# Performance work log

Hardware: AMD Instinct MI355X
Metric: run time of the kernel (lower is better)

## Reference

```python
import jax, jax.numpy as jnp
import numpy as np

E, K = 16, 4          # n_experts, top_k
C, H = 2048, 3584     # d_model, ffn_hidden
B, T = 2, 512
STD = 0.02


def setup_inputs() -> dict:
    key = jax.random.key(0)
    ks = jax.random.split(key, 5)
    x = jax.random.normal(ks[0], (B, T, C), jnp.float32)
    W_up = jax.random.normal(ks[1], (E, H, C), jnp.float32) * STD
    W_gate = jax.random.normal(ks[2], (E, H, C), jnp.float32) * STD
    W_down = jax.random.normal(ks[3], (E, C, H), jnp.float32) * STD
    gate_inp = jax.random.normal(ks[4], (E, C), jnp.float32) * STD
    return {"x": x, "W_up": W_up, "W_gate": W_gate, "W_down": W_down,
            "gate_inp": gate_inp}


def reference(x, W_up, W_gate, W_down, gate_inp):
    # x: [B, T, C]
    b, t, c = x.shape
    xf = x.reshape(b * t, c)                                  # [N, C]
    logits = xf @ gate_inp.T                                  # [N, E]
    topv, topi = jax.lax.top_k(logits, K)                     # [N, K]
    w = jax.nn.softmax(topv.astype(jnp.float32), axis=-1).astype(x.dtype)
    n = xf.shape[0]
    # Dense combine weights: zero for unselected experts -> identical math
    # to the original per-token gather, without the [N,K,H,C] blowup.
    dense_w = jnp.zeros((n, E), x.dtype).at[jnp.arange(n)[:, None], topi].set(w)
    u = jnp.einsum('nc,ehc->neh', xf, W_up)                   # [N, E, H]
    g = jnp.einsum('nc,ehc->neh', xf, W_gate)                 # [N, E, H]
    h = jax.nn.silu(g) * u                                    # SwiGLU
    y = jnp.einsum('neh,ech,ne->nc', h, W_down, dense_w)      # weighted combine
    return y.reshape(b, t, c)
```

## Files before the change

kernel.cpp:

```cpp
#include <hip/hip_runtime.h>
#include <math.h>

#define NTOK   1024
#define EXP    16
#define TOPK   4
#define DMODEL 2048
#define DFFN   3584
#define HT_TILES 56
#define CT_TILES 32
#define NSLOT  4096
#define MCH    64
#define NCHMAX 80

typedef __attribute__((ext_vector_type(8))) short bf16x8;
typedef __attribute__((ext_vector_type(4))) float f32x4;

#define O_COUNTS 0
#define O_BASE   256
#define O_CURSOR 512
#define O_CHT    1024
#define O_TOPI   4096
#define O_TOPW   (O_TOPI + 16384)
#define O_TOK    (O_TOPW + 16384)
#define O_WGT    (O_TOK + 16384)
#define O_SLOTNK (O_WGT + 16384)
#define O_XG     (O_SLOTNK + 16384)
#define O_HBUF   (O_XG + (size_t)NSLOT*DMODEL*2)

#define VMW(N) asm volatile("s_waitcnt vmcnt(" #N ")" ::: "memory")
#define LKW0() asm volatile("s_waitcnt lgkmcnt(0)" ::: "memory")
#define BAR()  __builtin_amdgcn_s_barrier()

__device__ __forceinline__ unsigned short f2b_rne(float f) {
  unsigned u = __builtin_bit_cast(unsigned, f);
  u += 0x7FFFu + ((u >> 16) & 1u);
  return (unsigned short)(u >> 16);
}
__device__ __forceinline__ float b2f(unsigned short h) {
  unsigned u = ((unsigned)h) << 16;
  return __builtin_bit_cast(float, u);
}
__device__ __forceinline__ unsigned pk2(float lo, float hi) {
  unsigned r;
  asm("v_cvt_pk_bf16_f32 %0, %1, %2" : "=v"(r) : "v"(lo), "v"(hi));
  return r;
}
__device__ __forceinline__ bf16x8 pack8(float4 a, float4 b) {
  union { unsigned u[4]; bf16x8 v; } r;
  r.u[0] = pk2(a.x, a.y); r.u[1] = pk2(a.z, a.w);
  r.u[2] = pk2(b.x, b.y); r.u[3] = pk2(b.z, b.w);
  return r.v;
}

__device__ __forceinline__ void gl16(const unsigned short* g, unsigned short* l) {
  __builtin_amdgcn_global_load_lds(
      (const __attribute__((address_space(1))) void*)g,
      (__attribute__((address_space(3))) void*)l, 16, 0, 0);
}

__device__ __forceinline__ bf16x8 ld_frag(const unsigned short* lds, int row, int chunk) {
  return *(const bf16x8*)(lds + row*64 + ((chunk ^ (row & 7)) * 8));
}

__global__ void k_zero(int* counts, int* cursor) {
  int t = threadIdx.x;
  if (t < EXP) { counts[t] = 0; cursor[t] = 0; }
}

__global__ void k_gate(const float* __restrict__ x, const float* __restrict__ gi,
                       int* __restrict__ topi, float* __restrict__ topw,
                       int* __restrict__ counts) {
  int n = blockIdx.x;
  int lane = threadIdx.x & 63, wave = threadIdx.x >> 6;
  __shared__ float lg[EXP];
  const float4* xr = (const float4*)(x + (size_t)n * DMODEL);
  #pragma unroll
  for (int i = 0; i < 4; ++i) {
    int e = wave * 4 + i;
    const float4* gr = (const float4*)(gi + (size_t)e * DMODEL);
    float s = 0.f;
    #pragma unroll
    for (int j = 0; j < 8; ++j) {
      float4 a = xr[j*64 + lane];
      float4 b = gr[j*64 + lane];
      s += a.x*b.x + a.y*b.y + a.z*b.z + a.w*b.w;
    }
    #pragma unroll
    for (int off = 32; off; off >>= 1) s += __shfl_xor(s, off);
    if (lane == 0) lg[e] = s;
  }
  __syncthreads();
  if (threadIdx.x == 0) {
    float v[EXP];
    #pragma unroll
    for (int j = 0; j < EXP; ++j) v[j] = lg[j];
    int bi[TOPK]; float bv[TOPK];
    #pragma unroll
    for (int k = 0; k < TOPK; ++k) {
      float best = -3.4e38f; int bidx = 0;
      for (int j = 0; j < EXP; ++j) if (v[j] > best) { best = v[j]; bidx = j; }
      bv[k] = best; bi[k] = bidx; v[bidx] = -3.4e38f;
    }
    float m = bv[0], ss = 0.f, w[TOPK];
    #pragma unroll
    for (int k = 0; k < TOPK; ++k) { w[k] = expf(bv[k] - m); ss += w[k]; }
    #pragma unroll
    for (int k = 0; k < TOPK; ++k) {
      topi[n*TOPK + k] = bi[k];
      topw[n*TOPK + k] = w[k] / ss;
      atomicAdd(&counts[bi[k]], 1);
    }
  }
}

__global__ void k_prefix(const int* __restrict__ counts, int* __restrict__ basep,
                         int* __restrict__ chtab) {
  if (threadIdx.x == 0) {
    int acc = 0;
    for (int e = 0; e < EXP; ++e) { basep[e] = acc; acc += counts[e]; }
    int c = 0;
    for (int e = 0; e < EXP; ++e) {
      int nm = (counts[e] + MCH - 1) / MCH;
      for (int m = 0; m < nm; ++m) { chtab[1 + c] = (e << 8) | m; ++c; }
    }
    chtab[0] = c;
    for (; c < NCHMAX; ++c) chtab[1 + c] = -1;
  }
}

__global__ void k_scatter(const int* __restrict__ topi, const float* __restrict__ topw,
                          const int* __restrict__ basep, int* __restrict__ cursor,
                          int* __restrict__ tok, float* __restrict__ wgt,
                          int* __restrict__ slotnk) {
  int n = blockIdx.x * blockDim.x + threadIdx.x;
  if (n >= NTOK) return;
  #pragma unroll
  for (int k = 0; k < TOPK; ++k) {
    int e = topi[n*TOPK + k];
    int pos = atomicAdd(&cursor[e], 1);
    int slot = basep[e] + pos;
    tok[slot] = n;
    wgt[slot] = topw[n*TOPK + k];
    slotnk[n*TOPK + k] = slot;
  }
}

__global__ void k_gather(const float* __restrict__ x, const int* __restrict__ tok,
                         unsigned short* __restrict__ xg) {
  int slot = blockIdx.x;
  int t = tok[slot];
  int c0 = threadIdx.x * 8;
  const float* src = x + (size_t)t * DMODEL + c0;
  float4 a = *(const float4*)(src);
  float4 b = *(const float4*)(src + 4);
  uint4 o = {pk2(a.x, a.y), pk2(a.z, a.w), pk2(b.x, b.y), pk2(b.z, b.w)};
  *(uint4*)(xg + (size_t)slot * DMODEL + c0) = o;
}

#define UG_STEP(XSC, XSN, PC, PN, KC) do {                                     \
    BAR();                                                                     \
    int kn_ = (KC) + 1; if (kn_ > DMODEL/64 - 1) kn_ = DMODEL/64 - 1;          \
    const float* pu_ = wu_row + kn_*64;                                        \
    const float* pg_ = wg_row + kn_*64;                                        \
    float4 r0_ = *(const float4*)(pu_);                                        \
    float4 r1_ = *(const float4*)(pu_ + 4);                                    \
    float4 r2_ = *(const float4*)(pu_ + 32);                                   \
    float4 r3_ = *(const float4*)(pu_ + 36);                                   \
    float4 r4_ = *(const float4*)(pg_);                                        \
    float4 r5_ = *(const float4*)(pg_ + 4);                                    \
    float4 r6_ = *(const float4*)(pg_ + 32);                                   \
    float4 r7_ = *(const float4*)(pg_ + 36);                                   \
    _Pragma("unroll")                                                          \
    for (int i_ = 0; i_ < 2; ++i_)                                             \
      gl16(bx[i_] + kn_*64, (XSN) + (wave*2 + i_)*8*64);                       \
    VMW(10);                                                                   \
    BAR();                                                                     \
    __builtin_amdgcn_s_setprio(1);                                             \
    _Pragma("unroll")                                                          \
    for (int kk_ = 0; kk_ < 2; ++kk_) {                                        \
      int chunk_ = kk_*4 + (lane >> 4);                                        \
      _Pragma("unroll")                                                        \
      for (int t_ = 0; t_ < 4; ++t_) {                                         \
        bf16x8 a_ = ld_frag((XSC), t_*16 + col, chunk_);                       \
        ua[t_] = __builtin_amdgcn_mfma_f32_16x16x32_bf16(a_, PC[kk_],   ua[t_], 0, 0, 0); \
        ga[t_] = __builtin_amdgcn_mfma_f32_16x16x32_bf16(a_, PC[2+kk_], ga[t_], 0, 0, 0); \
      }                                                                        \
    }                                                                          \
    __builtin_amdgcn_s_setprio(0);                                             \
    VMW(2);                                                                    \
    PN[0] = pack8(r0_, r1_); PN[1] = pack8(r2_, r3_);                          \
    PN[2] = pack8(r4_, r5_); PN[3] = pack8(r6_, r7_);                          \
  } while (0)

__global__ __launch_bounds__(256, 4) void k_upgate(
    const unsigned short* __restrict__ xg,
    const float* __restrict__ Wu, const float* __restrict__ Wg,
    const int* __restrict__ counts, const int* __restrict__ basep,
    const int* __restrict__ chtab, const float* __restrict__ wgt,
    unsigned short* __restrict__ hbuf) {
  int bid = blockIdx.x;
  int lb  = (bid & 7) * (NCHMAX*HT_TILES/8) + (bid >> 3);
  int cid = lb % NCHMAX, ht = lb / NCHMAX;
  int ent = chtab[1 + cid];
  if (ent < 0) return;
  int e = ent >> 8, mch = ent & 255;
  int n_e = counts[e], base_e = basep[e], mstart = mch * MCH;

  __shared__ unsigned short xs[2][64*64];
  __shared__ float swgt[MCH];

  int tid = threadIdx.x;
  int lane = tid & 63, wave = tid >> 6;
  int col = lane & 15;
  int kgrp = (lane >> 4) * 8;
  const float* wu_row = Wu + ((size_t)e * DFFN + (size_t)(ht*64 + wave*16 + col)) * DMODEL + kgrp;
  const float* wg_row = Wg + ((size_t)e * DFFN + (size_t)(ht*64 + wave*16 + col)) * DMODEL + kgrp;

  int xrow_lo = lane >> 3;
  int xpc     = lane & 7;
  int swz     = (xpc ^ xrow_lo) * 8;

  const unsigned short* bx[2];
  #pragma unroll
  for (int i = 0; i < 2; ++i) {
    int row = (wave*2 + i)*8 + xrow_lo;
    int slotr = base_e + mstart + row;
    if (slotr > NSLOT-1) slotr = NSLOT-1;
    bx[i] = xg + (size_t)slotr*DMODEL + swz;
  }

  if (tid < MCH) {
    int r = mstart + tid;
    swgt[tid] = (r < n_e) ? wgt[base_e + r] : 0.f;
  }
  LKW0();

  bf16x8 pA[4], pB[4];
  {
    const float* pu_ = wu_row;
    const float* pg_ = wg_row;
    float4 r0 = *(const float4*)(pu_);
    float4 r1 = *(const float4*)(pu_ + 4);
    float4 r2 = *(const float4*)(pu_ + 32);
    float4 r3 = *(const float4*)(pu_ + 36);
    float4 r4 = *(const float4*)(pg_);
    float4 r5 = *(const float4*)(pg_ + 4);
    float4 r6 = *(const float4*)(pg_ + 32);
    float4 r7 = *(const float4*)(pg_ + 36);
    #pragma unroll
    for (int i = 0; i < 2; ++i)
      gl16(bx[i], &xs[0][(wave*2 + i)*8*64]);
    VMW(2);
    pA[0] = pack8(r0, r1); pA[1] = pack8(r2, r3);
    pA[2] = pack8(r4, r5); pA[3] = pack8(r6, r7);
  }

  f32x4 ua[4], ga[4];
  #pragma unroll
  for (int t = 0; t < 4; ++t) { f32x4 z = {0.f,0.f,0.f,0.f}; ua[t] = z; ga[t] = z; }

  #pragma unroll 1
  for (int kc = 0; kc < DMODEL/64; kc += 2) {
    UG_STEP(xs[0], xs[1], pA, pB, kc);
    UG_STEP(xs[1], xs[0], pB, pA, kc + 1);
  }

  #pragma unroll
  for (int t = 0; t < 4; ++t)
    #pragma unroll
    for (int r = 0; r < 4; ++r) {
      int ml = t*16 + (lane >> 4)*4 + r;
      if (mstart + ml < n_e) {
        float u = ua[t][r], g = ga[t][r];
        float hv = u * (g / (1.f + expf(-g))) * swgt[ml];
        int slot = base_e + mstart + ml;
        hbuf[(size_t)slot*DFFN + ht*64 + wave*16 + col] = f2b_rne(hv);
      }
    }
}

#define DN_STEP(XSC, XSN, PC, PN, KC) do {                                     \
    BAR();                                                                     \
    int kn_ = (KC) + 1; if (kn_ > DFFN/64 - 1) kn_ = DFFN/64 - 1;              \
    const float* pd_ = wd_row + kn_*64;                                        \
    float4 r0_ = *(const float4*)(pd_);                                        \
    float4 r1_ = *(const float4*)(pd_ + 4);                                    \
    float4 r2_ = *(const float4*)(pd_ + 32);                                   \
    float4 r3_ = *(const float4*)(pd_ + 36);                                   \
    _Pragma("unroll")                                                          \
    for (int i_ = 0; i_ < 2; ++i_)                                             \
      gl16(bh[i_] + kn_*64, (XSN) + (wave*2 + i_)*8*64);                       \
    VMW(6);                                                                    \
    BAR();                                                                     \
    __builtin_amdgcn_s_setprio(1);                                             \
    _Pragma("unroll")                                                          \
    for (int kk_ = 0; kk_ < 2; ++kk_) {                                        \
      int chunk_ = kk_*4 + (lane >> 4);                                        \
      _Pragma("unroll")                                                        \
      for (int t_ = 0; t_ < 4; ++t_) {                                         \
        bf16x8 a_ = ld_frag((XSC), t_*16 + col, chunk_);                       \
        acc[t_] = __builtin_amdgcn_mfma_f32_16x16x32_bf16(a_, PC[kk_], acc[t_], 0, 0, 0); \
      }                                                                        \
    }                                                                          \
    __builtin_amdgcn_s_setprio(0);                                             \
    VMW(2);                                                                    \
    PN[0] = pack8(r0_, r1_); PN[1] = pack8(r2_, r3_);                          \
  } while (0)

__global__ __launch_bounds__(256, 4) void k_down(
    const unsigned short* __restrict__ hbuf, const float* __restrict__ Wd,
    const int* __restrict__ counts, const int* __restrict__ basep,
    const int* __restrict__ chtab,
    unsigned short* __restrict__ ypart) {
  int bid = blockIdx.x;
  int lb  = (bid & 7) * (NCHMAX*CT_TILES/8) + (bid >> 3);
  int cid = lb % NCHMAX, ct = lb / NCHMAX;
  int ent = chtab[1 + cid];
  if (ent < 0) return;
  int e = ent >> 8, mch = ent & 255;
  int n_e = counts[e], base_e = basep[e], mstart = mch * MCH;

  __shared__ unsigned short hs[2][64*64];

  int tid = threadIdx.x;
  int lane = tid & 63, wave = tid >> 6;
  int col = lane & 15;
  int kgrp = (lane >> 4) * 8;
  const float* wd_row = Wd + ((size_t)e * DMODEL + (size_t)(ct*64 + wave*16 + col)) * DFFN + kgrp;

  int xrow_lo = lane >> 3;
  int xpc     = lane & 7;
  int swz     = (xpc ^ xrow_lo) * 8;

  const unsigned short* bh[2];
  #pragma unroll
  for (int i = 0; i < 2; ++i) {
    int row = (wave*2 + i)*8 + xrow_lo;
    int slotr = base_e + mstart + row;
    if (slotr > NSLOT-1) slotr = NSLOT-1;
    bh[i] = hbuf + (size_t)slotr*DFFN + swz;
  }

  bf16x8 pA[2], pB[2];
  {
    const float* pd_ = wd_row;
    float4 r0 = *(const float4*)(pd_);
    float4 r1 = *(const float4*)(pd_ + 4);
    float4 r2 = *(const float4*)(pd_ + 32);
    float4 r3 = *(const float4*)(pd_ + 36);
    #pragma unroll
    for (int i = 0; i < 2; ++i)
      gl16(bh[i], &hs[0][(wave*2 + i)*8*64]);
    VMW(2);
    pA[0] = pack8(r0, r1); pA[1] = pack8(r2, r3);
  }

  f32x4 acc[4];
  #pragma unroll
  for (int t = 0; t < 4; ++t) { f32x4 z = {0.f,0.f,0.f,0.f}; acc[t] = z; }

  #pragma unroll 1
  for (int hc = 0; hc < DFFN/64; hc += 2) {
    DN_STEP(hs[0], hs[1], pA, pB, hc);
    DN_STEP(hs[1], hs[0], pB, pA, hc + 1);
  }

  #pragma unroll
  for (int t = 0; t < 4; ++t)
    #pragma unroll
    for (int r = 0; r < 4; ++r) {
      int ml = t*16 + (lane >> 4)*4 + r;
      if (mstart + ml < n_e) {
        int slot = base_e + mstart + ml;
        ypart[(size_t)slot*DMODEL + ct*64 + wave*16 + col] = f2b_rne(acc[t][r]);
      }
    }
}

__global__ void k_combine(const unsigned short* __restrict__ ypart,
                          const int* __restrict__ slotnk, float* __restrict__ out) {
  int n = blockIdx.x, tid = threadIdx.x;
  int c0 = tid * 8;
  float acc[8] = {0.f,0.f,0.f,0.f,0.f,0.f,0.f,0.f};
  #pragma unroll
  for (int k = 0; k < TOPK; ++k) {
    int slot = slotnk[n*TOPK + k];
    uint4 v = *(const uint4*)(ypart + (size_t)slot*DMODEL + c0);
    const unsigned short* p = (const unsigned short*)&v;
    #pragma unroll
    for (int j = 0; j < 8; ++j) acc[j] += b2f(p[j]);
  }
  float4 o0 = {acc[0], acc[1], acc[2], acc[3]};
  float4 o1 = {acc[4], acc[5], acc[6], acc[7]};
  *(float4*)(out + (size_t)n*DMODEL + c0)     = o0;
  *(float4*)(out + (size_t)n*DMODEL + c0 + 4) = o1;
}

extern "C" void kernel_launch(void* const* d_in, const int* in_sizes, int n_in,
                              void* d_out, int out_size, void* d_ws, size_t ws_size,
                              hipStream_t stream) {
  const float* x     = (const float*)d_in[0];
  const float* W_up  = (const float*)d_in[1];
  const float* W_gt  = (const float*)d_in[2];
  const float* W_dn  = (const float*)d_in[3];
  const float* g_in  = (const float*)d_in[4];
  float* out = (float*)d_out;
  char* ws = (char*)d_ws;

  int*   counts = (int*)(ws + O_COUNTS);
  int*   basep  = (int*)(ws + O_BASE);
  int*   cursor = (int*)(ws + O_CURSOR);
  int*   chtab  = (int*)(ws + O_CHT);
  int*   topi   = (int*)(ws + O_TOPI);
  float* topw   = (float*)(ws + O_TOPW);
  int*   tok    = (int*)(ws + O_TOK);
  float* wgt    = (float*)(ws + O_WGT);
  int*   slotnk = (int*)(ws + O_SLOTNK);
  unsigned short* xg    = (unsigned short*)(ws + O_XG);
  unsigned short* hbuf  = (unsigned short*)(ws + O_HBUF);
  unsigned short* ypart = xg;

  k_zero   <<<1, 64, 0, stream>>>(counts, cursor);
  k_gate   <<<NTOK, 256, 0, stream>>>(x, g_in, topi, topw, counts);
  k_prefix <<<1, 64, 0, stream>>>(counts, basep, chtab);
  k_scatter<<<4, 256, 0, stream>>>(topi, topw, basep, cursor, tok, wgt, slotnk);
  k_gather <<<NSLOT, 256, 0, stream>>>(x, tok, xg);
  k_upgate <<<NCHMAX*HT_TILES, 256, 0, stream>>>(xg, W_up, W_gt, counts, basep, chtab, wgt, hbuf);
  k_down   <<<NCHMAX*CT_TILES, 256, 0, stream>>>(hbuf, W_dn, counts, basep, chtab, ypart);
  k_combine<<<NTOK, 256, 0, stream>>>(ypart, slotnk, out);
}
```

Baseline: 916.9 us.

## Load activation fragments directly from global into registers, dropping LDS staging and barriers

Both grouped GEMM kernels (up/gate and down) no longer stage the token-activation tile in LDS through global_load_lds with barriers. Each lane now loads its MFMA A fragments straight from global memory into registers, double-buffered at a 32-wide K step. Launch bounds go from 4 to 3 blocks per CU to make room for the extra registers. This removes barrier and LDS traffic, but the four waves of a block now each reload the same activation rows, which adds L2/global traffic and uses smaller, less coalesced loads.

```diff
diff --git a/kernel.cpp b/kernel.cpp
--- a/kernel.cpp
+++ b/kernel.cpp
@@ -27,10 +27,6 @@
 #define O_XG     (O_SLOTNK + 16384)
 #define O_HBUF   (O_XG + (size_t)NSLOT*DMODEL*2)
 
-#define VMW(N) asm volatile("s_waitcnt vmcnt(" #N ")" ::: "memory")
-#define LKW0() asm volatile("s_waitcnt lgkmcnt(0)" ::: "memory")
-#define BAR()  __builtin_amdgcn_s_barrier()
-
 __device__ __forceinline__ unsigned short f2b_rne(float f) {
   unsigned u = __builtin_bit_cast(unsigned, f);
   u += 0x7FFFu + ((u >> 16) & 1u);
@@ -50,16 +46,6 @@
   r.u[0] = pk2(a.x, a.y); r.u[1] = pk2(a.z, a.w);
   r.u[2] = pk2(b.x, b.y); r.u[3] = pk2(b.z, b.w);
   return r.v;
-}
-
-__device__ __forceinline__ void gl16(const unsigned short* g, unsigned short* l) {
-  __builtin_amdgcn_global_load_lds(
-      (const __attribute__((address_space(1))) void*)g,
-      (__attribute__((address_space(3))) void*)l, 16, 0, 0);
-}
-
-__device__ __forceinline__ bf16x8 ld_frag(const unsigned short* lds, int row, int chunk) {
-  return *(const bf16x8*)(lds + row*64 + ((chunk ^ (row & 7)) * 8));
 }
 
 __global__ void k_zero(int* counts, int* cursor) {
@@ -157,42 +143,26 @@
   *(uint4*)(xg + (size_t)slot * DMODEL + c0) = o;
 }
 
-#define UG_STEP(XSC, XSN, PC, PN, KC) do {                                     \
-    BAR();                                                                     \
-    int kn_ = (KC) + 1; if (kn_ > DMODEL/64 - 1) kn_ = DMODEL/64 - 1;          \
-    const float* pu_ = wu_row + kn_*64;                                        \
-    const float* pg_ = wg_row + kn_*64;                                        \
-    float4 r0_ = *(const float4*)(pu_);                                        \
-    float4 r1_ = *(const float4*)(pu_ + 4);                                    \
-    float4 r2_ = *(const float4*)(pu_ + 32);                                   \
-    float4 r3_ = *(const float4*)(pu_ + 36);                                   \
-    float4 r4_ = *(const float4*)(pg_);                                        \
-    float4 r5_ = *(const float4*)(pg_ + 4);                                    \
-    float4 r6_ = *(const float4*)(pg_ + 32);                                   \
-    float4 r7_ = *(const float4*)(pg_ + 36);                                   \
+#define UG_STEP(AC, AN, PUC, PGC, PUN, PGN, KN) do {                           \
+    int o_ = (KN) * 32;                                                        \
+    AN[0] = *(const bf16x8*)(ax[0] + o_);                                      \
+    AN[1] = *(const bf16x8*)(ax[1] + o_);                                      \
+    AN[2] = *(const bf16x8*)(ax[2] + o_);                                      \
+    AN[3] = *(const bf16x8*)(ax[3] + o_);                                      \
+    float4 u0_ = *(const float4*)(wu + o_);                                    \
+    float4 u1_ = *(const float4*)(wu + o_ + 4);                                \
+    float4 g0_ = *(const float4*)(wg + o_);                                    \
+    float4 g1_ = *(const float4*)(wg + o_ + 4);                                \
     _Pragma("unroll")                                                          \
-    for (int i_ = 0; i_ < 2; ++i_)                                             \
-      gl16(bx[i_] + kn_*64, (XSN) + (wave*2 + i_)*8*64);                       \
-    VMW(10);                                                                   \
-    BAR();                                                                     \
-    __builtin_amdgcn_s_setprio(1);                                             \
-    _Pragma("unroll")                                                          \
-    for (int kk_ = 0; kk_ < 2; ++kk_) {                                        \
-      int chunk_ = kk_*4 + (lane >> 4);                                        \
-      _Pragma("unroll")                                                        \
-      for (int t_ = 0; t_ < 4; ++t_) {                                         \
-        bf16x8 a_ = ld_frag((XSC), t_*16 + col, chunk_);                       \
-        ua[t_] = __builtin_amdgcn_mfma_f32_16x16x32_bf16(a_, PC[kk_],   ua[t_], 0, 0, 0); \
-        ga[t_] = __builtin_amdgcn_mfma_f32_16x16x32_bf16(a_, PC[2+kk_], ga[t_], 0, 0, 0); \
-      }                                                                        \
+    for (int t_ = 0; t_ < 4; ++t_) {                                           \
+      ua[t_] = __builtin_amdgcn_mfma_f32_16x16x32_bf16(AC[t_], PUC, ua[t_], 0, 0, 0); \
+      ga[t_] = __builtin_amdgcn_mfma_f32_16x16x32_bf16(AC[t_], PGC, ga[t_], 0, 0, 0); \
     }                                                                          \
-    __builtin_amdgcn_s_setprio(0);                                             \
-    VMW(2);                                                                    \
-    PN[0] = pack8(r0_, r1_); PN[1] = pack8(r2_, r3_);                          \
-    PN[2] = pack8(r4_, r5_); PN[3] = pack8(r6_, r7_);                          \
+    PUN = pack8(u0_, u1_);                                                     \
+    PGN = pack8(g0_, g1_);                                                     \
   } while (0)
 
-__global__ __launch_bounds__(256, 4) void k_upgate(
+__global__ __launch_bounds__(256, 3) void k_upgate(
     const unsigned short* __restrict__ xg,
     const float* __restrict__ Wu, const float* __restrict__ Wg,
     const int* __restrict__ counts, const int* __restrict__ basep,
@@ -200,59 +170,38 @@
     unsigned short* __restrict__ hbuf) {
   int bid = blockIdx.x;
   int lb  = (bid & 7) * (NCHMAX*HT_TILES/8) + (bid >> 3);
-  int cid = lb % NCHMAX, ht = lb / NCHMAX;
+  int ht  = lb / NCHMAX, cid = lb % NCHMAX;
   int ent = chtab[1 + cid];
   if (ent < 0) return;
   int e = ent >> 8, mch = ent & 255;
   int n_e = counts[e], base_e = basep[e], mstart = mch * MCH;
 
-  __shared__ unsigned short xs[2][64*64];
-  __shared__ float swgt[MCH];
-
   int tid = threadIdx.x;
   int lane = tid & 63, wave = tid >> 6;
-  int col = lane & 15;
-  int kgrp = (lane >> 4) * 8;
-  const float* wu_row = Wu + ((size_t)e * DFFN + (size_t)(ht*64 + wave*16 + col)) * DMODEL + kgrp;
-  const float* wg_row = Wg + ((size_t)e * DFFN + (size_t)(ht*64 + wave*16 + col)) * DMODEL + kgrp;
-
-  int xrow_lo = lane >> 3;
-  int xpc     = lane & 7;
-  int swz     = (xpc ^ xrow_lo) * 8;
-
-  const unsigned short* bx[2];
-  #pragma unroll
-  for (int i = 0; i < 2; ++i) {
-    int row = (wave*2 + i)*8 + xrow_lo;
-    int slotr = base_e + mstart + row;
+  int col  = lane & 15;
+  int krow = lane >> 4;
+
+  const unsigned short* ax[4];
+  #pragma unroll
+  for (int t = 0; t < 4; ++t) {
+    int slotr = base_e + mstart + t*16 + col;
     if (slotr > NSLOT-1) slotr = NSLOT-1;
-    bx[i] = xg + (size_t)slotr*DMODEL + swz;
-  }
-
-  if (tid < MCH) {
-    int r = mstart + tid;
-    swgt[tid] = (r < n_e) ? wgt[base_e + r] : 0.f;
-  }
-  LKW0();
-
-  bf16x8 pA[4], pB[4];
+    ax[t] = xg + (size_t)slotr*DMODEL + krow*8;
+  }
+  const float* wu = Wu + ((size_t)e*DFFN + (size_t)(ht*64 + wave*16 + col))*DMODEL + krow*8;
+  const float* wg = Wg + ((size_t)e*DFFN + (size_t)(ht*64 + wave*16 + col))*DMODEL + krow*8;
+
+  bf16x8 a0[4], a1[4], pu0, pg0, pu1, pg1;
   {
-    const float* pu_ = wu_row;
-    const float* pg_ = wg_row;
-    float4 r0 = *(const float4*)(pu_);
-    float4 r1 = *(const float4*)(pu_ + 4);
-    float4 r2 = *(const float4*)(pu_ + 32);
-    float4 r3 = *(const float4*)(pu_ + 36);
-    float4 r4 = *(const float4*)(pg_);
-    float4 r5 = *(const float4*)(pg_ + 4);
-    float4 r6 = *(const float4*)(pg_ + 32);
-    float4 r7 = *(const float4*)(pg_ + 36);
-    #pragma unroll
-    for (int i = 0; i < 2; ++i)
-      gl16(bx[i], &xs[0][(wave*2 + i)*8*64]);
-    VMW(2);
-    pA[0] = pack8(r0, r1); pA[1] = pack8(r2, r3);
-    pA[2] = pack8(r4, r5); pA[3] = pack8(r6, r7);
+    a0[0] = *(const bf16x8*)(ax[0]);
+    a0[1] = *(const bf16x8*)(ax[1]);
+    a0[2] = *(const bf16x8*)(ax[2]);
+    a0[3] = *(const bf16x8*)(ax[3]);
+    float4 u0 = *(const float4*)(wu);
+    float4 u1 = *(const float4*)(wu + 4);
+    float4 g0 = *(const float4*)(wg);
+    float4 g1 = *(const float4*)(wg + 4);
+    pu0 = pack8(u0, u1); pg0 = pack8(g0, g1);
   }
 
   f32x4 ua[4], ga[4];
@@ -260,99 +209,77 @@
   for (int t = 0; t < 4; ++t) { f32x4 z = {0.f,0.f,0.f,0.f}; ua[t] = z; ga[t] = z; }
 
   #pragma unroll 1
-  for (int kc = 0; kc < DMODEL/64; kc += 2) {
-    UG_STEP(xs[0], xs[1], pA, pB, kc);
-    UG_STEP(xs[1], xs[0], pB, pA, kc + 1);
+  for (int kc = 0; kc < DMODEL/32; kc += 2) {
+    UG_STEP(a0, a1, pu0, pg0, pu1, pg1, kc + 1);
+    int kn2 = kc + 2; if (kn2 > DMODEL/32 - 1) kn2 = DMODEL/32 - 1;
+    UG_STEP(a1, a0, pu1, pg1, pu0, pg0, kn2);
   }
 
   #pragma unroll
   for (int t = 0; t < 4; ++t)
     #pragma unroll
     for (int r = 0; r < 4; ++r) {
-      int ml = t*16 + (lane >> 4)*4 + r;
+      int ml = t*16 + krow*4 + r;
       if (mstart + ml < n_e) {
+        float w = wgt[base_e + mstart + ml];
         float u = ua[t][r], g = ga[t][r];
-        float hv = u * (g / (1.f + expf(-g))) * swgt[ml];
+        float hv = u * (g / (1.f + expf(-g))) * w;
         int slot = base_e + mstart + ml;
         hbuf[(size_t)slot*DFFN + ht*64 + wave*16 + col] = f2b_rne(hv);
       }
     }
 }
 
-#define DN_STEP(XSC, XSN, PC, PN, KC) do {                                     \
-    BAR();                                                                     \
-    int kn_ = (KC) + 1; if (kn_ > DFFN/64 - 1) kn_ = DFFN/64 - 1;              \
-    const float* pd_ = wd_row + kn_*64;                                        \
-    float4 r0_ = *(const float4*)(pd_);                                        \
-    float4 r1_ = *(const float4*)(pd_ + 4);                                    \
-    float4 r2_ = *(const float4*)(pd_ + 32);                                   \
-    float4 r3_ = *(const float4*)(pd_ + 36);                                   \
+#define DN_STEP(AC, AN, PDC, PDN, KN) do {                                     \
+    int o_ = (KN) * 32;                                                        \
+    AN[0] = *(const bf16x8*)(ah[0] + o_);                                      \
+    AN[1] = *(const bf16x8*)(ah[1] + o_);                                      \
+    AN[2] = *(const bf16x8*)(ah[2] + o_);                                      \
+    AN[3] = *(const bf16x8*)(ah[3] + o_);                                      \
+    float4 d0_ = *(const float4*)(wd + o_);                                    \
+    float4 d1_ = *(const float4*)(wd + o_ + 4);                                \
     _Pragma("unroll")                                                          \
-    for (int i_ = 0; i_ < 2; ++i_)                                             \
-      gl16(bh[i_] + kn_*64, (XSN) + (wave*2 + i_)*8*64);                       \
-    VMW(6);                                                                    \
-    BAR();                                                                     \
-    __builtin_amdgcn_s_setprio(1);                                             \
-    _Pragma("unroll")                                                          \
-    for (int kk_ = 0; kk_ < 2; ++kk_) {                                        \
-      int chunk_ = kk_*4 + (lane >> 4);                                        \
-      _Pragma("unroll")                                                        \
-      for (int t_ = 0; t_ < 4; ++t_) {                                         \
-        bf16x8 a_ = ld_frag((XSC), t_*16 + col, chunk_);                       \
-        acc[t_] = __builtin_amdgcn_mfma_f32_16x16x32_bf16(a_, PC[kk_], acc[t_], 0, 0, 0); \
-      }                                                                        \
-    }                                                                          \
-    __builtin_amdgcn_s_setprio(0);                                             \
-    VMW(2);                                                                    \
-    PN[0] = pack8(r0_, r1_); PN[1] = pack8(r2_, r3_);                          \
+    for (int t_ = 0; t_ < 4; ++t_)                                             \
+      acc[t_] = __builtin_amdgcn_mfma_f32_16x16x32_bf16(AC[t_], PDC, acc[t_], 0, 0, 0); \
+    PDN = pack8(d0_, d1_);                                                     \
   } while (0)
 
-__global__ __launch_bounds__(256, 4) void k_down(
+__global__ __launch_bounds__(256, 3) void k_down(
     const unsigned short* __restrict__ hbuf, const float* __restrict__ Wd,
     const int* __restrict__ counts, const int* __restrict__ basep,
     const int* __restrict__ chtab,
     unsigned short* __restrict__ ypart) {
   int bid = blockIdx.x;
   int lb  = (bid & 7) * (NCHMAX*CT_TILES/8) + (bid >> 3);
-  int cid = lb % NCHMAX, ct = lb / NCHMAX;
+  int ct  = lb / NCHMAX, cid = lb % NCHMAX;
   int ent = chtab[1 + cid];
   if (ent < 0) return;
   int e = ent >> 8, mch = ent & 255;
   int n_e = counts[e], base_e = basep[e], mstart = mch * MCH;
 
-  __shared__ unsigned short hs[2][64*64];
-
   int tid = threadIdx.x;
   int lane = tid & 63, wave = tid >> 6;
-  int col = lane & 15;
-  int kgrp = (lane >> 4) * 8;
-  const float* wd_row = Wd + ((size_t)e * DMODEL + (size_t)(ct*64 + wave*16 + col)) * DFFN + kgrp;
-
-  int xrow_lo = lane >> 3;
-  int xpc     = lane & 7;
-  int swz     = (xpc ^ xrow_lo) * 8;
-
-  const unsigned short* bh[2];
-  #pragma unroll
-  for (int i = 0; i < 2; ++i) {
-    int row = (wave*2 + i)*8 + xrow_lo;
-    int slotr = base_e + mstart + row;
+  int col  = lane & 15;
+  int krow = lane >> 4;
+
+  const unsigned short* ah[4];
+  #pragma unroll
+  for (int t = 0; t < 4; ++t) {
+    int slotr = base_e + mstart + t*16 + col;
     if (slotr > NSLOT-1) slotr = NSLOT-1;
-    bh[i] = hbuf + (size_t)slotr*DFFN + swz;
-  }
-
-  bf16x8 pA[2], pB[2];
+    ah[t] = hbuf + (size_t)slotr*DFFN + krow*8;
+  }
+  const float* wd = Wd + ((size_t)e*DMODEL + (size_t)(ct*64 + wave*16 + col))*DFFN + krow*8;
+
+  bf16x8 a0[4], a1[4], pd0, pd1;
   {
-    const float* pd_ = wd_row;
-    float4 r0 = *(const float4*)(pd_);
-    float4 r1 = *(const float4*)(pd_ + 4);
-    float4 r2 = *(const float4*)(pd_ + 32);
-    float4 r3 = *(const float4*)(pd_ + 36);
-    #pragma unroll
-    for (int i = 0; i < 2; ++i)
-      gl16(bh[i], &hs[0][(wave*2 + i)*8*64]);
-    VMW(2);
-    pA[0] = pack8(r0, r1); pA[1] = pack8(r2, r3);
+    a0[0] = *(const bf16x8*)(ah[0]);
+    a0[1] = *(const bf16x8*)(ah[1]);
+    a0[2] = *(const bf16x8*)(ah[2]);
+    a0[3] = *(const bf16x8*)(ah[3]);
+    float4 d0 = *(const float4*)(wd);
+    float4 d1 = *(const float4*)(wd + 4);
+    pd0 = pack8(d0, d1);
   }
 
   f32x4 acc[4];
@@ -360,16 +287,17 @@
   for (int t = 0; t < 4; ++t) { f32x4 z = {0.f,0.f,0.f,0.f}; acc[t] = z; }
 
   #pragma unroll 1
-  for (int hc = 0; hc < DFFN/64; hc += 2) {
-    DN_STEP(hs[0], hs[1], pA, pB, hc);
-    DN_STEP(hs[1], hs[0], pB, pA, hc + 1);
+  for (int hc = 0; hc < DFFN/32; hc += 2) {
+    DN_STEP(a0, a1, pd0, pd1, hc + 1);
+    int kn2 = hc + 2; if (kn2 > DFFN/32 - 1) kn2 = DFFN/32 - 1;
+    DN_STEP(a1, a0, pd1, pd0, kn2);
   }
 
   #pragma unroll
   for (int t = 0; t < 4; ++t)
     #pragma unroll
     for (int r = 0; r < 4; ++r) {
-      int ml = t*16 + (lane >> 4)*4 + r;
+      int ml = t*16 + krow*4 + r;
       if (mstart + ml < n_e) {
         int slot = base_e + mstart + ml;
         ypart[(size_t)slot*DMODEL + ct*64 + wave*16 + col] = f2b_rne(acc[t][r]);
```

Measured after the change: 1.739 ms. 1.9x slower.
